# Kernel optimization log

Hardware: AMD Instinct MI355X
Metric: run time of the kernel (lower is better)

## Reference

```python
import jax, jax.numpy as jnp
import numpy as np

SCALING = 2.0  # alpha / r = 128 / 64


def setup_inputs() -> dict:
    key = jax.random.key(0)
    k1, k2, k3, k4, k5 = jax.random.split(key, 5)
    B, S, DIN, DOUT, R = 4, 2048, 4096, 4096, 64
    x = jax.random.normal(k1, (B, S, DIN), dtype=jnp.float32)
    # int8 quantized weight codes in [-127, 127] (stored as int32 for portability)
    qweight = jax.random.randint(k2, (DOUT, DIN), -127, 128, dtype=jnp.int32)
    # per-output-row absmax dequant scale (already divided by 127)
    scale = jax.random.uniform(k3, (DOUT, 1), dtype=jnp.float32, minval=0.005, maxval=0.02)
    lora_A = jax.random.normal(k4, (R, DIN), dtype=jnp.float32) * 0.02
    lora_B = jax.random.normal(k5, (DOUT, R), dtype=jnp.float32) * 0.02
    return {"x": x, "qweight": qweight, "scale": scale, "lora_A": lora_A, "lora_B": lora_B}


def reference(x, qweight, scale, lora_A, lora_B):
    # inline int8 dequant: w[o,i] = code[o,i] * scale[o]
    w = qweight.astype(x.dtype) * scale  # [DOUT, DIN]
    base = jnp.einsum('bsi,oi->bso', x, w)
    # low-rank LoRA path: (x @ A^T) @ B^T, scaled
    xa = jnp.einsum('bsi,ri->bsr', x, lora_A)       # [B,S,R]
    lora = jnp.einsum('bsr,or->bso', xa, lora_B)    # [B,S,DOUT]
    return base + SCALING * lora
```

## Files before the change

### kernel.cpp

```cpp
#include <hip/hip_runtime.h>
#include <hip/hip_bf16.h>
#include <stdint.h>


typedef __bf16 bf16x8 __attribute__((ext_vector_type(8)));
typedef float f32x4 __attribute__((ext_vector_type(4)));
typedef int i32x4 __attribute__((ext_vector_type(4)));

#define DIN   4096
#define DOUT  4096
#define MTOT  8192
#define RNK   64
#define NT    64

__device__ inline void gload_lds16(const void* g, void* l) {
  __builtin_amdgcn_global_load_lds((const __attribute__((address_space(1))) void*)g,
                                   (__attribute__((address_space(3))) void*)l,
                                   16, 0, 0);
}

__global__ __launch_bounds__(256) void prep_kernel(const float* __restrict__ x,
                                                   const int* __restrict__ qw,
                                                   const float* __restrict__ lA,
                                                   const float* __restrict__ lB,
                                                   signed char* __restrict__ Xi8,
                                                   float* __restrict__ tstep,
                                                   signed char* __restrict__ Wi8,
                                                   signed char* __restrict__ Ai8,
                                                   float* __restrict__ astep,
                                                   __bf16* __restrict__ Blt) {
  const int bid = blockIdx.x, t = threadIdx.x;
  const float* src = nullptr;
  signed char* dst = nullptr;
  float* stp = nullptr;
  int row = 0;
  if (bid < 8192) { src = x; dst = Xi8; stp = tstep; row = bid; }
  else if (bid < 8256) { src = lA; dst = Ai8; stp = astep; row = bid - 8192; }
  if (src) {
    const float4* xr = (const float4*)(src + (size_t)row * DIN);
    float4 v[4];
    float m = 0.f;
#pragma unroll
    for (int s = 0; s < 4; ++s) {
      v[s] = xr[t + s * 256];
      m = fmaxf(m, fmaxf(fmaxf(fabsf(v[s].x), fabsf(v[s].y)),
                         fmaxf(fabsf(v[s].z), fabsf(v[s].w))));
    }
#pragma unroll
    for (int off = 32; off > 0; off >>= 1) m = fmaxf(m, __shfl_xor(m, off));
    __shared__ float wm[4];
    if ((t & 63) == 0) wm[t >> 6] = m;
    __syncthreads();
    m = fmaxf(fmaxf(wm[0], wm[1]), fmaxf(wm[2], wm[3]));
    m = fmaxf(m, 1e-30f);
    const float rs = 127.0f / m;
    int* orow = (int*)(dst + (size_t)row * DIN);
#pragma unroll
    for (int s = 0; s < 4; ++s) {
      float e[4] = {v[s].x, v[s].y, v[s].z, v[s].w};
      union { signed char c[4]; int i; } p;
#pragma unroll
      for (int j = 0; j < 4; ++j) {
        int q = __float2int_rn(e[j] * rs);
        q = q > 127 ? 127 : (q < -127 ? -127 : q);
        p.c[j] = (signed char)q;
      }
      orow[t + s * 256] = p.i;
    }
    if (t == 0) stp[row] = m * (1.0f / 127.0f);
  } else if (bid < 8512) {
    int i = (bid - 8256) * 256 + t;
    float4 v = ((const float4*)lB)[i];
    union { __bf16 h[4]; uint64_t u; } p;
    p.h[0] = (__bf16)(2.0f * v.x); p.h[1] = (__bf16)(2.0f * v.y);
    p.h[2] = (__bf16)(2.0f * v.z); p.h[3] = (__bf16)(2.0f * v.w);
    ((uint64_t*)Blt)[i] = p.u;
  } else {
    int i = (bid - 8512) * 256 + t;
    int4 v = ((const int4*)qw)[i];
    union { signed char c[4]; int i; } p;
    p.c[0] = (signed char)v.x; p.c[1] = (signed char)v.y;
    p.c[2] = (signed char)v.z; p.c[3] = (signed char)v.w;
    ((int*)Wi8)[i] = p.i;
  }
}

__global__ __launch_bounds__(256) void lora_xa_kernel(const signed char* __restrict__ Xi8,
                                                      const float* __restrict__ tstep,
                                                      const signed char* __restrict__ Ai8,
                                                      const float* __restrict__ astep,
                                                      __bf16* __restrict__ xa) {
  __shared__ i32x4 red[4][64][4];
  const int w = threadIdx.x >> 6, lane = threadIdx.x & 63;
  const int rowbase = blockIdx.x * 16;
  i32x4 acc[4] = {};
  const int k00 = w * 1024 + (lane >> 4) * 16;
  const signed char* xrow = Xi8 + (size_t)(rowbase + (lane & 15)) * DIN + k00;
  const signed char* ab = Ai8 + (size_t)(lane & 15) * DIN + k00;
#pragma unroll 4
  for (int k = 0; k < 1024; k += 64) {
    i32x4 af = *(const i32x4*)(xrow + k);
#pragma unroll
    for (int ni = 0; ni < 4; ++ni) {
      i32x4 bv = *(const i32x4*)(ab + (size_t)ni * 16 * DIN + k);
      acc[ni] = __builtin_amdgcn_mfma_i32_16x16x64_i8(af, bv, acc[ni], 0, 0, 0);
    }
  }
#pragma unroll
  for (int ni = 0; ni < 4; ++ni) red[w][lane][ni] = acc[ni];
  __syncthreads();
  if (w == 0) {
    f32x4 tm = *(const f32x4*)&tstep[rowbase + (lane >> 4) * 4];
#pragma unroll
    for (int ni = 0; ni < 4; ++ni) {
      i32x4 s = red[0][lane][ni];
#pragma unroll
      for (int u = 1; u < 4; ++u) s += red[u][lane][ni];
      const int col = ni * 16 + (lane & 15);
      const float as = astep[col];
#pragma unroll
      for (int j = 0; j < 4; ++j) {
        int row = rowbase + (lane >> 4) * 4 + j;
        xa[(size_t)row * RNK + col] = (__bf16)((float)s[j] * tm[j] * as);
      }
    }
  }
}

__global__ __launch_bounds__(512, 1) void gemm_i8_kernel(const signed char* __restrict__ Xi8,
                                                         const signed char* __restrict__ Wi8,
                                                         const float* __restrict__ scale,
                                                         const float* __restrict__ tstep,
                                                         const __bf16* __restrict__ xa,
                                                         const __bf16* __restrict__ Blt,
                                                         float* __restrict__ out) {
  extern __shared__ char smem[];
  const int tid = threadIdx.x;
  const int lane = tid & 63;
  const int w = tid >> 6;
  const int wr = w >> 2;
  const int wc = w & 3;

  const int swz = (blockIdx.x & 7) * 64 + (blockIdx.x >> 3);
  const int bx = swz & 15;
  const int by = swz >> 4;
  const size_t bm = (size_t)by * 256, bn = (size_t)bx * 256;

  const int rc = ((lane >> 4) ^ ((lane >> 1) & 3)) << 4;
  const int srow = tid >> 2;
  const int scol = ((tid & 3) ^ ((tid >> 3) & 3)) << 4;

  auto SH = [&](const signed char* g, size_t r0, int srct, int ldsoff) {
    gload_lds16(g + (r0 + srow) * (size_t)4096 + srct * 64 + scol,
                smem + ldsoff + tid * 16);
  };
  auto stage = [&](int srct) {
    if (srct >= NT) return;
    int b = (srct % 5) * 32768;
    SH(Xi8, bm, srct, b); SH(Xi8, bm + 128, srct, b + 8192);
    SH(Wi8, bn, srct, b + 16384); SH(Wi8, bn + 128, srct, b + 24576);
  };

  i32x4 aP[4], bP[4], aQ[4], bQ[4], a2[4];
  i32x4 acc[8][4] = {};

  stage(0); stage(1); stage(2);
  asm volatile("s_waitcnt vmcnt(0)" ::: "memory");
  __builtin_amdgcn_s_barrier();
  {
    const int ab0 = wr * 8192 + (lane & 15) * 64 + rc;
    const int bb0 = 16384 + (wc >> 1) * 8192 + (wc & 1) * 4096 + (lane & 15) * 64 + rc;
#pragma unroll
    for (int mi = 0; mi < 4; ++mi) aP[mi] = *(const i32x4*)(smem + ab0 + mi * 1024);
#pragma unroll
    for (int ni = 0; ni < 4; ++ni) bP[ni] = *(const i32x4*)(smem + bb0 + ni * 1024);
  }

  auto body = [&](int kt, auto& ac, auto& bc, auto& an, auto& bn, bool prefetch) {
    const int bufb = (kt % 5) * 32768;
    const int ab = bufb + wr * 8192 + (lane & 15) * 64 + rc;
#pragma unroll
    for (int mi = 0; mi < 4; ++mi)
      a2[mi] = *(const i32x4*)(smem + ab + 4096 + mi * 1024);
#pragma unroll
    for (int mi = 0; mi < 4; ++mi)
#pragma unroll
      for (int ni = 0; ni < 4; ++ni)
        acc[mi][ni] = __builtin_amdgcn_mfma_i32_16x16x64_i8(ac[mi], bc[ni], acc[mi][ni], 0, 0, 0);
    if (prefetch) {
      const int nbufb = ((kt + 1) % 5) * 32768;
      const int nab = nbufb + wr * 8192 + (lane & 15) * 64 + rc;
      const int nbb = nbufb + 16384 + (wc >> 1) * 8192 + (wc & 1) * 4096 + (lane & 15) * 64 + rc;
#pragma unroll
      for (int mi = 0; mi < 4; ++mi) an[mi] = *(const i32x4*)(smem + nab + mi * 1024);
#pragma unroll
      for (int ni = 0; ni < 4; ++ni) bn[ni] = *(const i32x4*)(smem + nbb + ni * 1024);
    }
#pragma unroll
    for (int mi = 0; mi < 4; ++mi)
#pragma unroll
      for (int ni = 0; ni < 4; ++ni)
        acc[4 + mi][ni] = __builtin_amdgcn_mfma_i32_16x16x64_i8(a2[mi], bc[ni], acc[4 + mi][ni], 0, 0, 0);
  };

  for (int kt = 0; kt < NT; kt += 2) {
    stage(kt + 3); stage(kt + 4);
    body(kt, aP, bP, aQ, bQ, true);
    body(kt + 1, aQ, bQ, aP, bP, kt + 2 < NT);
    __builtin_amdgcn_sched_barrier(0);
    asm volatile("s_waitcnt vmcnt(0)" ::: "memory");
    __builtin_amdgcn_s_barrier();
  }

  const int sl_row = lane >> 3;
  const int sl_col = ((lane & 7) ^ (lane >> 3)) << 4;
  auto SBF = [&](const __bf16* g, size_t r0, int ldsoff) {
    char* d0 = smem + ldsoff + w * 2048 + lane * 16;
#pragma unroll
    for (int s = 0; s < 2; ++s) {
      const int rl = (w * 2 + s) * 8 + sl_row;
      gload_lds16((const char*)g + (r0 + rl) * 128 + sl_col, d0 + s * 1024);
    }
  };
  SBF(xa, bm, 0); SBF(xa, bm + 128, 16384);
  SBF(Blt, bn, 32768); SBF(Blt, bn + 128, 49152);

  float sc[4];
#pragma unroll
  for (int ni = 0; ni < 4; ++ni)
    sc[ni] = scale[bn + wc * 64 + ni * 16 + (lane & 15)];
  f32x4 tm[8];
#pragma unroll
  for (int mi = 0; mi < 8; ++mi)
    tm[mi] = *(const f32x4*)&tstep[bm + wr * 128 + mi * 16 + (lane >> 4) * 4];

  asm volatile("s_waitcnt vmcnt(0)" ::: "memory");
  __builtin_amdgcn_s_barrier();

  const int cx0 = ((lane >> 4) << 4) ^ ((lane & 7) << 4);
  const int cx1 = (64 | ((lane >> 4) << 4)) ^ ((lane & 7) << 4);
  const int abE = wr * 16384 + (lane & 15) * 128;
  const int bbE = 32768 + (wc >> 1) * 16384 + ((wc & 1) * 64 + (lane & 15)) * 128;

  bf16x8 bl0[4], bl1[4];
#pragma unroll
  for (int ni = 0; ni < 4; ++ni) {
    bl0[ni] = *(const bf16x8*)(smem + bbE + ni * 2048 + cx0);
    bl1[ni] = *(const bf16x8*)(smem + bbE + ni * 2048 + cx1);
  }
#pragma unroll
  for (int mi = 0; mi < 8; ++mi) {
    bf16x8 ax0 = *(const bf16x8*)(smem + abE + mi * 2048 + cx0);
    bf16x8 ax1 = *(const bf16x8*)(smem + abE + mi * 2048 + cx1);
    const size_t row = bm + wr * 128 + mi * 16 + (lane >> 4) * 4;
#pragma unroll
    for (int ni = 0; ni < 4; ++ni) {
      f32x4 l = {0.f, 0.f, 0.f, 0.f};
      l = __builtin_amdgcn_mfma_f32_16x16x32_bf16(ax0, bl0[ni], l, 0, 0, 0);
      l = __builtin_amdgcn_mfma_f32_16x16x32_bf16(ax1, bl1[ni], l, 0, 0, 0);
      const size_t col = bn + wc * 64 + ni * 16 + (lane & 15);
#pragma unroll
      for (int j = 0; j < 4; ++j)
        out[(row + j) * DOUT + col] = (float)acc[mi][ni][j] * (sc[ni] * tm[mi][j]) + l[j];
    }
  }
}

extern "C" void kernel_launch(void* const* d_in, const int* in_sizes, int n_in,
                              void* d_out, int out_size, void* d_ws, size_t ws_size,
                              hipStream_t stream) {
  const float* x = (const float*)d_in[0];
  const int* qw = (const int*)d_in[1];
  const float* scale = (const float*)d_in[2];
  const float* lA = (const float*)d_in[3];
  const float* lB = (const float*)d_in[4];
  float* out = (float*)d_out;

  char* ws = (char*)d_ws;
  signed char* Xi8 = (signed char*)ws;
  signed char* Wi8 = (signed char*)(ws + 33554432);
  __bf16* xa    = (__bf16*)(ws + 50331648);
  signed char* Ai8 = (signed char*)(ws + 51380224);
  __bf16* Blt   = (__bf16*)(ws + 51904512);
  float* tstep  = (float*)(ws + 52428800);
  float* astep  = (float*)(ws + 52461568);

  hipFuncSetAttribute((const void*)gemm_i8_kernel,
                      hipFuncAttributeMaxDynamicSharedMemorySize, 163840);

  prep_kernel<<<24896, 256, 0, stream>>>(x, qw, lA, lB, Xi8, tstep, Wi8, Ai8, astep, Blt);
  lora_xa_kernel<<<MTOT / 16, 256, 0, stream>>>(Xi8, tstep, Ai8, astep, xa);
  gemm_i8_kernel<<<(MTOT / 256) * (DOUT / 256), 512, 163840, stream>>>(
      Xi8, Wi8, scale, tstep, xa, Blt, out);
}
```

Measured before the change: 205.1 us.

## Load int8 A operand directly into registers, stage only W through LDS

The X (A) tiles no longer go through shared memory. Each wave now loads its A fragments straight from global memory into registers, prefetching one k-step ahead. Only the weight tiles are staged into LDS, using a 4-deep ring with a barrier after every k-step. This cuts LDS use from 160KB to 64KB and removes LDS reads for A, which may allow more blocks per CU. The cost is that the four column-waves sharing a row group each fetch the same A data from global/L2, with only 64-byte contiguous segments per row, and barriers become twice as frequent.

```diff
diff --git a/kernel.cpp b/kernel.cpp
--- a/kernel.cpp
+++ b/kernel.cpp
@@ -150,68 +150,57 @@
   const int srow = tid >> 2;
   const int scol = ((tid & 3) ^ ((tid >> 3) & 3)) << 4;
 
-  auto SH = [&](const signed char* g, size_t r0, int srct, int ldsoff) {
-    gload_lds16(g + (r0 + srow) * (size_t)4096 + srct * 64 + scol,
-                smem + ldsoff + tid * 16);
-  };
-  auto stage = [&](int srct) {
-    if (srct >= NT) return;
-    int b = (srct % 5) * 32768;
-    SH(Xi8, bm, srct, b); SH(Xi8, bm + 128, srct, b + 8192);
-    SH(Wi8, bn, srct, b + 16384); SH(Wi8, bn + 128, srct, b + 24576);
-  };
-
-  i32x4 aP[4], bP[4], aQ[4], bQ[4], a2[4];
+  auto stageB = [&](int srct, int buf) {
+    int b = buf * 16384;
+    gload_lds16(Wi8 + (bn + srow) * (size_t)4096 + srct * 64 + scol,
+                smem + b + tid * 16);
+    gload_lds16(Wi8 + (bn + 128 + srow) * (size_t)4096 + srct * 64 + scol,
+                smem + b + 8192 + tid * 16);
+  };
+
+  const signed char* abase = Xi8 + (bm + wr * 128 + (lane & 15)) * (size_t)4096
+                                 + (lane >> 4) * 16;
+  auto aload = [&](int kt, i32x4 (&ar)[8]) {
+    const signed char* p = abase + kt * 64;
+#pragma unroll
+    for (int mi = 0; mi < 8; ++mi)
+      ar[mi] = *(const i32x4*)(p + (size_t)mi * 16 * 4096);
+  };
+
+  const int boff = (wc >> 1) * 8192 + (wc & 1) * 4096 + (lane & 15) * 64 + rc;
+
+  i32x4 aP[8], aQ[8];
   i32x4 acc[8][4] = {};
 
-  stage(0); stage(1); stage(2);
+  stageB(0, 0); stageB(1, 1); stageB(2, 2);
+  aload(0, aP);
   asm volatile("s_waitcnt vmcnt(0)" ::: "memory");
   __builtin_amdgcn_s_barrier();
-  {
-    const int ab0 = wr * 8192 + (lane & 15) * 64 + rc;
-    const int bb0 = 16384 + (wc >> 1) * 8192 + (wc & 1) * 4096 + (lane & 15) * 64 + rc;
-#pragma unroll
-    for (int mi = 0; mi < 4; ++mi) aP[mi] = *(const i32x4*)(smem + ab0 + mi * 1024);
-#pragma unroll
-    for (int ni = 0; ni < 4; ++ni) bP[ni] = *(const i32x4*)(smem + bb0 + ni * 1024);
-  }
-
-  auto body = [&](int kt, auto& ac, auto& bc, auto& an, auto& bn, bool prefetch) {
-    const int bufb = (kt % 5) * 32768;
-    const int ab = bufb + wr * 8192 + (lane & 15) * 64 + rc;
-#pragma unroll
-    for (int mi = 0; mi < 4; ++mi)
-      a2[mi] = *(const i32x4*)(smem + ab + 4096 + mi * 1024);
-#pragma unroll
-    for (int mi = 0; mi < 4; ++mi)
+
+  auto body = [&](int kt, i32x4 (&aC)[8], i32x4 (&aN)[8]) {
+    if (kt + 3 < NT) stageB(kt + 3, (kt + 3) & 3);
+    if (kt + 1 < NT) aload(kt + 1, aN);
+    const int bufb = (kt & 3) * 16384;
+    i32x4 b[4];
+#pragma unroll
+    for (int ni = 0; ni < 4; ++ni)
+      b[ni] = *(const i32x4*)(smem + bufb + boff + ni * 1024);
+#pragma unroll
+    for (int mi = 0; mi < 8; ++mi)
 #pragma unroll
       for (int ni = 0; ni < 4; ++ni)
-        acc[mi][ni] = __builtin_amdgcn_mfma_i32_16x16x64_i8(ac[mi], bc[ni], acc[mi][ni], 0, 0, 0);
-    if (prefetch) {
-      const int nbufb = ((kt + 1) % 5) * 32768;
-      const int nab = nbufb + wr * 8192 + (lane & 15) * 64 + rc;
-      const int nbb = nbufb + 16384 + (wc >> 1) * 8192 + (wc & 1) * 4096 + (lane & 15) * 64 + rc;
-#pragma unroll
-      for (int mi = 0; mi < 4; ++mi) an[mi] = *(const i32x4*)(smem + nab + mi * 1024);
-#pragma unroll
-      for (int ni = 0; ni < 4; ++ni) bn[ni] = *(const i32x4*)(smem + nbb + ni * 1024);
-    }
-#pragma unroll
-    for (int mi = 0; mi < 4; ++mi)
-#pragma unroll
-      for (int ni = 0; ni < 4; ++ni)
-        acc[4 + mi][ni] = __builtin_amdgcn_mfma_i32_16x16x64_i8(a2[mi], bc[ni], acc[4 + mi][ni], 0, 0, 0);
+        acc[mi][ni] = __builtin_amdgcn_mfma_i32_16x16x64_i8(aC[mi], b[ni], acc[mi][ni], 0, 0, 0);
+    __builtin_amdgcn_sched_barrier(0);
+    __builtin_amdgcn_s_barrier();
   };
 
   for (int kt = 0; kt < NT; kt += 2) {
-    stage(kt + 3); stage(kt + 4);
-    body(kt, aP, bP, aQ, bQ, true);
-    body(kt + 1, aQ, bQ, aP, bP, kt + 2 < NT);
-    __builtin_amdgcn_sched_barrier(0);
-    asm volatile("s_waitcnt vmcnt(0)" ::: "memory");
-    __builtin_amdgcn_s_barrier();
-  }
-
+    body(kt, aP, aQ);
+    body(kt + 1, aQ, aP);
+  }
+
+  asm volatile("s_waitcnt vmcnt(0)" ::: "memory");
+  __builtin_amdgcn_s_barrier();
   const int sl_row = lane >> 3;
   const int sl_col = ((lane & 7) ^ (lane >> 3)) << 4;
   auto SBF = [&](const __bf16* g, size_t r0, int ldsoff) {
@@ -286,10 +275,10 @@
   float* astep  = (float*)(ws + 52461568);
 
   hipFuncSetAttribute((const void*)gemm_i8_kernel,
-                      hipFuncAttributeMaxDynamicSharedMemorySize, 163840);
+                      hipFuncAttributeMaxDynamicSharedMemorySize, 65536);
 
   prep_kernel<<<24896, 256, 0, stream>>>(x, qw, lA, lB, Xi8, tstep, Wi8, Ai8, astep, Blt);
   lora_xa_kernel<<<MTOT / 16, 256, 0, stream>>>(Xi8, tstep, Ai8, astep, xa);
-  gemm_i8_kernel<<<(MTOT / 256) * (DOUT / 256), 512, 163840, stream>>>(
+  gemm_i8_kernel<<<(MTOT / 256) * (DOUT / 256), 512, 65536, stream>>>(
       Xi8, Wi8, scale, tstep, xa, Blt, out);
 }
```

Result: slower. 411.5 us (+100.7%).
